# Performance work log

Measured on AMD Instinct MI355X. Metric: run time of the kernel, lower is better.

The kernel has to match this reference:

```python
import jax, jax.numpy as jnp
import numpy as np


def setup_inputs() -> dict:
    key = jax.random.key(0)
    k1, k2 = jax.random.split(key)
    tensor_1 = jax.random.normal(k1, (8192, 256), dtype=jnp.float32)
    tensor_2 = jax.random.normal(k2, (16384, 256), dtype=jnp.float32)
    return {"tensor_1": tensor_1, "tensor_2": tensor_2}


def reference(tensor_1, tensor_2):
    # L2-normalize along the feature dim (matches torch .norm(dim=-1), no eps)
    n1 = tensor_1 / jnp.linalg.norm(tensor_1, axis=-1, keepdims=True)  # [N, d]
    n2 = tensor_2 / jnp.linalg.norm(tensor_2, axis=-1, keepdims=True)  # [M, d]
    cos_sim = jnp.einsum("nd,md->nm", n1, n2)  # [N, M] cosine similarity
    top3, _ = jax.lax.top_k(cos_sim, 3)        # [N, 3]
    return top3.mean(axis=-1)                  # [N]
```

## Files before the change

### kernel.cpp

```cpp
#include <hip/hip_runtime.h>
#include <hip/hip_bf16.h>
#include <stdint.h>

#define N1 8192
#define N2 16384
#define DIM 256
#define BM 256
#define CS 16
#define COLS (N2 / CS)
#define TC 32
#define NT (COLS / TC)
#define NPART CS

typedef short v8s  __attribute__((ext_vector_type(8)));
typedef float f32x4 __attribute__((ext_vector_type(4)));

#define GLD16(g, l)                                                                         \
  __builtin_amdgcn_global_load_lds((const __attribute__((address_space(1))) uint32_t*)(g),  \
                                   (__attribute__((address_space(3))) uint32_t*)(l), 16, 0, 0)

__device__ __forceinline__ void top3_insert(float v, float& t0, float& t1, float& t2) {
    float nt1 = __builtin_amdgcn_fmed3f(v, t0, t1);
    float nt2 = __builtin_amdgcn_fmed3f(v, t1, t2);
    t0 = fmaxf(t0, v);
    t1 = nt1;
    t2 = nt2;
}

__global__ __launch_bounds__(256) void normalize_kernel(
        const float* __restrict__ inA, const float* __restrict__ inB,
        __hip_bfloat16* __restrict__ outA, __hip_bfloat16* __restrict__ outB) {
    const int wave = threadIdx.x >> 6;
    const int lane = threadIdx.x & 63;
    const int rgrp = lane >> 4;
    const int li   = lane & 15;
    const int gr   = blockIdx.x * 16 + wave * 4 + rgrp;
    const float* in;
    __hip_bfloat16* out;
    int row;
    if (gr < N1) { in = inA; out = outA; row = gr; }
    else         { in = inB; out = outB; row = gr - N1; }
    const float* rp = in + (size_t)row * DIM + li * 4;
    float4 v[4];
    #pragma unroll
    for (int j = 0; j < 4; ++j) v[j] = *(const float4*)(rp + j * 64);
    float s = 0.f;
    #pragma unroll
    for (int j = 0; j < 4; ++j)
        s += v[j].x * v[j].x + v[j].y * v[j].y + v[j].z * v[j].z + v[j].w * v[j].w;
    #pragma unroll
    for (int off = 8; off; off >>= 1) s += __shfl_xor(s, off, 64);
    const float inv = 1.0f / sqrtf(s);
    __hip_bfloat16* wp = out + (size_t)row * DIM + li * 4;
    #pragma unroll
    for (int j = 0; j < 4; ++j) {
        __hip_bfloat16 o[4];
        o[0] = __float2bfloat16(v[j].x * inv);
        o[1] = __float2bfloat16(v[j].y * inv);
        o[2] = __float2bfloat16(v[j].z * inv);
        o[3] = __float2bfloat16(v[j].w * inv);
        *(uint2*)(wp + j * 64) = *(uint2*)o;
    }
}

__global__ __launch_bounds__(256, 2) void gemm_top3_kernel(
        const __hip_bfloat16* __restrict__ A, const __hip_bfloat16* __restrict__ B,
        float* __restrict__ partial) {
    __shared__ char smem[2 * 16384];

    const int tid  = threadIdx.x;
    const int wave = tid >> 6;
    const int lane = tid & 63;
    const int lo   = lane & 15;
    const int quad = lane >> 4;
    const int cs   = blockIdx.x & 15;
    const int rb   = blockIdx.x >> 4;
    const int row0 = rb * BM;

    v8s af[4][8];
    {
        const char* arow = (const char*)A + (size_t)(row0 + wave * 64 + lo) * 512 + quad * 16;
        #pragma unroll
        for (int rt = 0; rt < 4; ++rt)
            #pragma unroll
            for (int s = 0; s < 8; ++s) {
                v8s t = *(const v8s*)(arow + rt * 8192 + s * 64);
                asm("" : "=a"(af[rt][s]) : "0"(t));
            }
    }
    asm volatile("s_waitcnt vmcnt(0)" ::: "memory");

    const char* Bb = (const char*)B + (size_t)cs * COLS * 512;
    int gsrc[4];
    #pragma unroll
    for (int j = 0; j < 4; ++j) {
        const int col = j * 8 + wave * 2 + (lane >> 5);
        gsrc[j] = col * 512 + (((lane & 31) ^ (col & 7)) << 4);
    }

    int swz[8];
    #pragma unroll
    for (int s = 0; s < 8; ++s) swz[s] = (((s * 4 + quad) ^ (lo & 7)) << 4);
    const int bco0 = lo * 512;
    const int bco1 = (16 + lo) * 512;

    float t0[16], t1[16], t2[16];
    #pragma unroll
    for (int i = 0; i < 16; ++i) { t0[i] = -1e30f; t1[i] = -1e30f; t2[i] = -1e30f; }

    #pragma unroll
    for (int j = 0; j < 4; ++j)
        GLD16(Bb + gsrc[j], smem + j * 4096 + wave * 1024);
    #pragma unroll
    for (int j = 0; j < 4; ++j)
        GLD16(Bb + 16384 + gsrc[j], smem + 16384 + j * 4096 + wave * 1024);

    #define DO_TILE(BOFF, GATE4, stage_ok, src_off)                                        \
    {                                                                                      \
        if (GATE4) asm volatile("s_waitcnt vmcnt(4)" ::: "memory");                        \
        else       asm volatile("s_waitcnt vmcnt(0)" ::: "memory");                        \
        __builtin_amdgcn_s_barrier();                                                      \
        f32x4 acc[4][2];                                                                   \
        _Pragma("unroll")                                                                  \
        for (int rt = 0; rt < 4; ++rt) {                                                   \
            acc[rt][0] = (f32x4){0.f, 0.f, 0.f, 0.f};                                      \
            acc[rt][1] = (f32x4){0.f, 0.f, 0.f, 0.f};                                      \
        }                                                                                  \
        __builtin_amdgcn_s_setprio(1);                                                     \
        _Pragma("unroll")                                                                  \
        for (int s = 0; s < 8; ++s) {                                                      \
            v8s bf0 = *(const v8s*)(smem + (BOFF) + bco0 + swz[s]);                        \
            v8s bf1 = *(const v8s*)(smem + (BOFF) + bco1 + swz[s]);                        \
            _Pragma("unroll")                                                              \
            for (int rt = 0; rt < 4; ++rt) {                                               \
                asm("v_mfma_f32_16x16x32_bf16 %0, %1, %2, %0"                              \
                    : "+v"(acc[rt][0]) : "a"(af[rt][s]), "v"(bf0));                        \
                asm("v_mfma_f32_16x16x32_bf16 %0, %1, %2, %0"                              \
                    : "+v"(acc[rt][1]) : "a"(af[rt][s]), "v"(bf1));                        \
            }                                                                              \
        }                                                                                  \
        __builtin_amdgcn_s_setprio(0);                                                     \
        __builtin_amdgcn_s_barrier();                                                      \
        if (stage_ok) {                                                                    \
            const char* src = Bb + (size_t)(src_off);                                      \
            _Pragma("unroll")                                                              \
            for (int j = 0; j < 4; ++j)                                                    \
                GLD16(src + gsrc[j], smem + (BOFF) + j * 4096 + wave * 1024);              \
        }                                                                                  \
        _Pragma("unroll")                                                                  \
        for (int rt = 0; rt < 4; ++rt)                                                     \
            _Pragma("unroll")                                                              \
            for (int r = 0; r < 4; ++r) {                                                  \
                const int sl = rt * 4 + r;                                                 \
                top3_insert(acc[rt][0][r], t0[sl], t1[sl], t2[sl]);                        \
                top3_insert(acc[rt][1][r], t0[sl], t1[sl], t2[sl]);                        \
            }                                                                              \
    }

    for (int tt = 0; tt < NT / 2; ++tt) {
        const int te = 2 * tt;
        const bool st = (tt < NT / 2 - 1);
        DO_TILE(0,     true, st, (size_t)(te + 2) * 16384);
        DO_TILE(16384, st,   st, (size_t)(te + 3) * 16384);
    }
    #undef DO_TILE

    #pragma unroll
    for (int sl = 0; sl < 16; ++sl) {
        #pragma unroll
        for (int step = 1; step < 16; step <<= 1) {
            float b0 = __shfl_xor(t0[sl], step, 64);
            float b1 = __shfl_xor(t1[sl], step, 64);
            float b2 = __shfl_xor(t2[sl], step, 64);
            top3_insert(b0, t0[sl], t1[sl], t2[sl]);
            top3_insert(b1, t0[sl], t1[sl], t2[sl]);
            top3_insert(b2, t0[sl], t1[sl], t2[sl]);
        }
    }
    if (lo == 0) {
        #pragma unroll
        for (int rt = 0; rt < 4; ++rt)
            #pragma unroll
            for (int r = 0; r < 4; ++r) {
                const int row = row0 + wave * 64 + rt * 16 + quad * 4 + r;
                float* p = partial + ((size_t)row * NPART + cs) * 3;
                const int sl = rt * 4 + r;
                p[0] = t0[sl]; p[1] = t1[sl]; p[2] = t2[sl];
            }
    }
}

__global__ __launch_bounds__(256) void merge_kernel(
        const float* __restrict__ partial, float* __restrict__ out) {
    const int row = blockIdx.x * 256 + threadIdx.x;
    if (row >= N1) return;
    const float4* p = (const float4*)(partial + (size_t)row * NPART * 3);
    float t0 = -1e30f, t1 = -1e30f, t2 = -1e30f;
    #pragma unroll
    for (int i = 0; i < 12; ++i) {
        float4 v = p[i];
        top3_insert(v.x, t0, t1, t2);
        top3_insert(v.y, t0, t1, t2);
        top3_insert(v.z, t0, t1, t2);
        top3_insert(v.w, t0, t1, t2);
    }
    out[row] = (t0 + t1 + t2) * (1.0f / 3.0f);
}

extern "C" void kernel_launch(void* const* d_in, const int* in_sizes, int n_in,
                              void* d_out, int out_size, void* d_ws, size_t ws_size,
                              hipStream_t stream) {
    const float* tA = (const float*)d_in[0];
    const float* tB = (const float*)d_in[1];
    float* out = (float*)d_out;

    __hip_bfloat16* An = (__hip_bfloat16*)d_ws;
    __hip_bfloat16* Bn = An + (size_t)N1 * DIM;
    float* partial = (float*)(Bn + (size_t)N2 * DIM);

    normalize_kernel<<<(N1 + N2) / 16, 256, 0, stream>>>(tA, tB, An, Bn);
    gemm_top3_kernel<<<(N1 / BM) * CS, 256, 0, stream>>>(An, Bn, partial);
    merge_kernel<<<N1 / 256, 256, 0, stream>>>(partial, out);
}
```

Baseline: 138.2 us.

## Restructure B-tile pipeline: single barrier per tile, early prefetch, register double-buffered LDS reads

Changes the double-buffered LDS pipeline so each tile waits for all loads, runs one barrier, then immediately issues the global-to-LDS prefetch of the next tile into the other buffer before computing. Only one tile is prefetched ahead instead of two. It also drops the second barrier per tile and the wait after the A-fragment load. LDS fragment reads are software-pipelined two steps ahead in registers so MFMAs overlap ds_read latency. The risk is less prefetch distance (vmcnt(0) each tile), which may expose global-load latency.

```diff
diff --git a/kernel.cpp b/kernel.cpp
--- a/kernel.cpp
+++ b/kernel.cpp
@@ -88,7 +88,6 @@
                 asm("" : "=a"(af[rt][s]) : "0"(t));
             }
     }
-    asm volatile("s_waitcnt vmcnt(0)" ::: "memory");
 
     const char* Bb = (const char*)B + (size_t)cs * COLS * 512;
     int gsrc[4];
@@ -111,59 +110,61 @@
     #pragma unroll
     for (int j = 0; j < 4; ++j)
         GLD16(Bb + gsrc[j], smem + j * 4096 + wave * 1024);
-    #pragma unroll
-    for (int j = 0; j < 4; ++j)
-        GLD16(Bb + 16384 + gsrc[j], smem + 16384 + j * 4096 + wave * 1024);
-
-    #define DO_TILE(BOFF, GATE4, stage_ok, src_off)                                        \
-    {                                                                                      \
-        if (GATE4) asm volatile("s_waitcnt vmcnt(4)" ::: "memory");                        \
-        else       asm volatile("s_waitcnt vmcnt(0)" ::: "memory");                        \
-        __builtin_amdgcn_s_barrier();                                                      \
-        f32x4 acc[4][2];                                                                   \
-        _Pragma("unroll")                                                                  \
-        for (int rt = 0; rt < 4; ++rt) {                                                   \
-            acc[rt][0] = (f32x4){0.f, 0.f, 0.f, 0.f};                                      \
-            acc[rt][1] = (f32x4){0.f, 0.f, 0.f, 0.f};                                      \
-        }                                                                                  \
-        __builtin_amdgcn_s_setprio(1);                                                     \
-        _Pragma("unroll")                                                                  \
-        for (int s = 0; s < 8; ++s) {                                                      \
-            v8s bf0 = *(const v8s*)(smem + (BOFF) + bco0 + swz[s]);                        \
-            v8s bf1 = *(const v8s*)(smem + (BOFF) + bco1 + swz[s]);                        \
-            _Pragma("unroll")                                                              \
-            for (int rt = 0; rt < 4; ++rt) {                                               \
-                asm("v_mfma_f32_16x16x32_bf16 %0, %1, %2, %0"                              \
-                    : "+v"(acc[rt][0]) : "a"(af[rt][s]), "v"(bf0));                        \
-                asm("v_mfma_f32_16x16x32_bf16 %0, %1, %2, %0"                              \
-                    : "+v"(acc[rt][1]) : "a"(af[rt][s]), "v"(bf1));                        \
-            }                                                                              \
-        }                                                                                  \
-        __builtin_amdgcn_s_setprio(0);                                                     \
-        __builtin_amdgcn_s_barrier();                                                      \
-        if (stage_ok) {                                                                    \
-            const char* src = Bb + (size_t)(src_off);                                      \
-            _Pragma("unroll")                                                              \
-            for (int j = 0; j < 4; ++j)                                                    \
-                GLD16(src + gsrc[j], smem + (BOFF) + j * 4096 + wave * 1024);              \
-        }                                                                                  \
-        _Pragma("unroll")                                                                  \
-        for (int rt = 0; rt < 4; ++rt)                                                     \
-            _Pragma("unroll")                                                              \
-            for (int r = 0; r < 4; ++r) {                                                  \
-                const int sl = rt * 4 + r;                                                 \
-                top3_insert(acc[rt][0][r], t0[sl], t1[sl], t2[sl]);                        \
-                top3_insert(acc[rt][1][r], t0[sl], t1[sl], t2[sl]);                        \
-            }                                                                              \
-    }
-
-    for (int tt = 0; tt < NT / 2; ++tt) {
-        const int te = 2 * tt;
-        const bool st = (tt < NT / 2 - 1);
-        DO_TILE(0,     true, st, (size_t)(te + 2) * 16384);
-        DO_TILE(16384, st,   st, (size_t)(te + 3) * 16384);
+
+    #define RD(dst, S, BOFF)                                                   \
+        do {                                                                   \
+            (dst)[0] = *(const v8s*)(smem + (BOFF) + bco0 + swz[S]);           \
+            (dst)[1] = *(const v8s*)(smem + (BOFF) + bco1 + swz[S]);           \
+        } while (0)
+
+    #define DO_TILE(BOFF, OTHER, t)                                            \
+    {                                                                          \
+        asm volatile("s_waitcnt vmcnt(0)" ::: "memory");                       \
+        __builtin_amdgcn_s_barrier();                                          \
+        if ((t) + 1 < NT) {                                                    \
+            const char* src = Bb + (size_t)((t) + 1) * 16384;                  \
+            _Pragma("unroll")                                                  \
+            for (int j = 0; j < 4; ++j)                                        \
+                GLD16(src + gsrc[j], smem + (OTHER) + j * 4096 + wave * 1024); \
+        }                                                                      \
+        f32x4 acc[4][2];                                                       \
+        _Pragma("unroll")                                                      \
+        for (int rt = 0; rt < 4; ++rt) {                                       \
+            acc[rt][0] = (f32x4){0.f, 0.f, 0.f, 0.f};                          \
+            acc[rt][1] = (f32x4){0.f, 0.f, 0.f, 0.f};                          \
+        }                                                                      \
+        v8s bf[2][2];                                                          \
+        RD(bf[0], 0, BOFF);                                                    \
+        RD(bf[1], 1, BOFF);                                                    \
+        __builtin_amdgcn_s_setprio(1);                                         \
+        _Pragma("unroll")                                                      \
+        for (int s = 0; s < 8; ++s) {                                          \
+            _Pragma("unroll")                                                  \
+            for (int rt = 0; rt < 4; ++rt) {                                   \
+                asm("v_mfma_f32_16x16x32_bf16 %0, %1, %2, %0"                  \
+                    : "+v"(acc[rt][0]) : "a"(af[rt][s]), "v"(bf[s & 1][0]));   \
+                asm("v_mfma_f32_16x16x32_bf16 %0, %1, %2, %0"                  \
+                    : "+v"(acc[rt][1]) : "a"(af[rt][s]), "v"(bf[s & 1][1]));   \
+            }                                                                  \
+            if (s + 2 < 8) RD(bf[s & 1], s + 2, BOFF);                         \
+        }                                                                      \
+        __builtin_amdgcn_s_setprio(0);                                         \
+        _Pragma("unroll")                                                      \
+        for (int rt = 0; rt < 4; ++rt)                                         \
+            _Pragma("unroll")                                                  \
+            for (int r = 0; r < 4; ++r) {                                      \
+                const int sl = rt * 4 + r;                                     \
+                top3_insert(acc[rt][0][r], t0[sl], t1[sl], t2[sl]);            \
+                top3_insert(acc[rt][1][r], t0[sl], t1[sl], t2[sl]);            \
+            }                                                                  \
+    }
+
+    for (int tt = 0; tt < NT; tt += 2) {
+        DO_TILE(0,     16384, tt);
+        DO_TILE(16384, 0,     tt + 1);
     }
     #undef DO_TILE
+    #undef RD
 
     #pragma unroll
     for (int sl = 0; sl < 16; ++sl) {
```

Result: no change. 138.5 us (+0.2%).
